# Kernel tuning notes

Measured on AMD Instinct MI355X. Metric: run time of the kernel, lower is better.

## Reference

```python
import jax, jax.numpy as jnp
import numpy as np

B, C, T, N = 8, 128, 12, 4096
E_HALF = 131072
EPS = 1e-5


def _linear_params(key, fan_in, fan_out):
    kw, kb = jax.random.split(key)
    bound = 1.0 / np.sqrt(fan_in)
    W = jax.random.uniform(kw, (fan_in, fan_out), jnp.float32, -bound, bound)
    b = jax.random.uniform(kb, (fan_out,), jnp.float32, -bound, bound)
    return W, b


def setup_inputs() -> dict:
    key = jax.random.key(0)
    ks = jax.random.split(key, 10)
    h_in = jax.random.normal(ks[0], (B, C, T, N), jnp.float32)
    # symmetric edge list: random pairs + reverses + self loops
    u = jax.random.randint(ks[1], (E_HALF,), 0, N, jnp.int32)
    v = jax.random.randint(ks[2], (E_HALF,), 0, N, jnp.int32)
    loops = jnp.arange(N, dtype=jnp.int32)
    row = jnp.concatenate([u, v, loops])
    col = jnp.concatenate([v, u, loops])
    edge_index = jnp.stack([row, col])  # [2, E]
    Wq, bq = _linear_params(ks[3], C, C)
    Wk, bk = _linear_params(ks[4], C, C)
    Wv, bv = _linear_params(ks[5], C, C)
    W1, b1 = _linear_params(ks[6], 2 * C, 4 * C)
    W2, b2 = _linear_params(ks[7], 4 * C, C)
    W3, b3 = _linear_params(ks[8], C, 1)
    return dict(h_in=h_in, edge_index=edge_index, Wq=Wq, bq=bq, Wk=Wk, bk=bk,
                Wv=Wv, bv=bv, W1=W1, b1=b1, W2=W2, b2=b2, W3=W3, b3=b3)


def _masked_instance_norm(x, mask_f):
    # stats over the non-self-loop edges only (matching torch, where the MLP
    # only sees edge_index[:, non_self_loop_mask])
    cnt = mask_f.sum()
    mean = (x * mask_f).sum(0) / cnt
    var = (((x - mean) ** 2) * mask_f).sum(0) / cnt
    return (x - mean) / jnp.sqrt(var + EPS)


def _forward(h_in, edge_index, Wq, bq, Wk, bk, Wv, bv, W1, b1, W2, b2, W3, b3):
    # ---- TemporalAttention ----
    x = jnp.transpose(h_in, (0, 3, 2, 1))  # [B, N, T, C]
    q = x @ Wq + bq
    k = x @ Wk + bk
    v = x @ Wv + bv
    scores = jnp.einsum('bntc,bnsc->bnts', q, k) / (C ** 0.5)
    attn = jax.nn.softmax(scores, axis=-1)
    weighted = jnp.einsum('bnts,bnsc->bntc', attn, v)
    emb = weighted.sum(axis=2)          # [B, N, C]
    emb_mean = emb.mean(axis=0)         # [N, C]

    # ---- ExtractorMLP on non-self-loop edges ----
    row, col = edge_index[0], edge_index[1]
    self_loop = row == col
    mask_f = (~self_loop).astype(emb_mean.dtype)[:, None]  # [E, 1]
    f12 = jnp.concatenate([emb_mean[row], emb_mean[col]], axis=-1)  # [E, 2C]
    h = jax.nn.relu(_masked_instance_norm(f12 @ W1 + b1, mask_f))
    h = jax.nn.relu(_masked_instance_norm(h @ W2 + b2, mask_f))
    logits = h @ W3 + b3                 # [E, 1]

    # concrete_sample, eval mode (deterministic)
    att = jax.nn.sigmoid(logits)
    all_att = jnp.where(self_loop[:, None], 1.0, att)  # [E, 1]

    # ---- transpose + reorder_like: match each edge with its reverse ----
    M = jnp.max(edge_index) + 1
    fwd_key = row * M + col
    rev_key = col * M + row
    order = jnp.argsort(fwd_key)
    pos = jnp.searchsorted(fwd_key[order], rev_key)
    perm = order[pos]                    # index of reverse edge
    edge_att = (all_att + all_att[perm]) * 0.5
    return edge_att


def reference(h_in, edge_index, Wq, bq, Wk, bk, Wv, bv, W1, b1, W2, b2, W3, b3):
    return _forward(h_in, edge_index, Wq, bq, Wk, bk, Wv, bv, W1, b1, W2, b2, W3, b3)
```

## Files before the change

kernel.cpp:

```cpp
#include <hip/hip_runtime.h>
#include <hip/hip_bf16.h>

#define CC     128
#define TT     12
#define NNODE  4096
#define NE     266240
#define EHALF  131072
#define F1     512
#define EPS    1e-5f
#define RSQRTC 0.08838834764831845f
#define LOG2E  1.4426950408889634f
#define EBG    48
#define NBLKG2 5547
#define NF2B   87
#define ST     40

#define O_XWM   0ull
#define O_ICNT  524288ull
#define O_CNT   524416ull
#define O_T     528512ull
#define O_S     528640ull
#define O_T2    545024ull
#define O_GTB   561664ull
#define O_W0B   569856ull
#define O_WC1   569920ull
#define O_WC2   635456ull
#define O_B1C   700992ull
#define O_M1    701504ull
#define O_IS1   702016ull
#define O_M2    702528ull
#define O_AW    702656ull
#define O_W2T   702784ull
#define O_PB    735552ull
#define O_QB    1784128ull
#define O_PART  2832704ull
#define O_PART2 4252736ull
#define O_Z2    4275008ull

typedef __attribute__((ext_vector_type(8))) short bf16x8;
typedef __attribute__((ext_vector_type(4))) float f32x4;

__device__ inline float bfbits2f(unsigned int v) { return __uint_as_float(v << 16); }
__device__ inline unsigned short f2bf(float x) {
  union { __hip_bfloat16 h; unsigned short u; } cv;
  cv.h = __float2bfloat16(x);
  return cv.u;
}
__device__ inline float f4get(const float4& v, int k) {
  return k == 0 ? v.x : k == 1 ? v.y : k == 2 ? v.z : v.w;
}

__global__ __launch_bounds__(256) void k_setup(
    const float* __restrict__ Wq, const float* __restrict__ bq,
    const float* __restrict__ Wk, const float* __restrict__ Wv,
    const float* __restrict__ bv, const float* __restrict__ W1,
    const float* __restrict__ b1, const float* __restrict__ W2,
    const int* __restrict__ row, const int* __restrict__ col,
    unsigned short* __restrict__ Gtb, unsigned short* __restrict__ w0b,
    float* __restrict__ Wc1, float* __restrict__ Wc2, float* __restrict__ b1c,
    unsigned short* __restrict__ W2T, int* __restrict__ cnt, int* __restrict__ icnt) {
  __shared__ float wvr[CC];
  __shared__ int h[NNODE];
  const int blk = blockIdx.x, tid = threadIdx.x;
  if (blk < 128) {
    if (tid < 128) {
      int i = blk, j = tid;
      float acc = 0.f;
      for (int co = 0; co < CC; ++co) acc = fmaf(Wq[i*CC+co], Wk[j*CC+co], acc);
      Gtb[j*CC + i] = f2bf(acc);
      if (j == 0) {
        float a = 0.f;
        for (int co = 0; co < CC; ++co) a = fmaf(Wk[i*CC+co], bq[co], a);
        w0b[i] = f2bf(a);
      }
    }
  } else if (blk < 256) {
    const int c = blk - 128;
    if (tid < CC) wvr[tid] = Wv[(size_t)c*CC + tid];
    __syncthreads();
    for (int hh = 0; hh < 2; ++hh) {
      int f = hh*256 + tid;
      float a1 = 0.f, a2 = 0.f;
      for (int j = 0; j < CC; ++j) {
        float wv = wvr[j];
        a1 = fmaf(wv, W1[(size_t)j*F1 + f], a1);
        a2 = fmaf(wv, W1[(size_t)(CC + j)*F1 + f], a2);
      }
      Wc1[(size_t)c*F1 + f] = a1;
      Wc2[(size_t)c*F1 + f] = a2;
    }
    if (c == 0) {
      for (int hh = 0; hh < 2; ++hh) {
        int f = hh*256 + tid;
        float s = b1[f];
        for (int j = 0; j < CC; ++j)
          s = fmaf(12.f*bv[j], W1[(size_t)j*F1 + f] + W1[(size_t)(CC + j)*F1 + f], s);
        b1c[f] = s;
      }
    }
  } else if (blk < 384) {
    const int n = blk - 256;
    for (int k = tid; k < F1; k += 256)
      W2T[(size_t)n*F1 + k] = f2bf(W2[(size_t)k*CC + n]);
  } else {
    for (int i = tid; i < NNODE; i += 256) h[i] = 0;
    __syncthreads();
    int lc = 0;
    const int base = (blk - 384) << 12;
    for (int i = tid; i < 4096; i += 256) {
      int e = base + i;
      int r = row[e], c = col[e];
      if (r != c) { atomicAdd(&h[r], 1); ++lc; }
    }
    #pragma unroll
    for (int d = 1; d < 64; d <<= 1) lc += __shfl_xor(lc, d);
    __syncthreads();
    for (int i = tid; i < NNODE; i += 256) { int v = h[i]; if (v) atomicAdd(&cnt[i], v); }
    if ((tid & 63) == 0) atomicAdd(icnt, lc);
  }
}

__global__ __launch_bounds__(512, 6) void k_attn(
    const float* __restrict__ h_in,
    const unsigned short* __restrict__ Gtb,
    const unsigned short* __restrict__ w0b,
    float* __restrict__ xwm) {
  __shared__ unsigned short xs[96*128];
  __shared__ unsigned short ys[97*128];
  const int tid = threadIdx.x;
  const int b  = blockIdx.x & 7;
  const int n0 = (blockIdx.x >> 3) << 3;

  const int w = tid >> 6, lane = tid & 63;
  const int l15 = lane & 15, l4 = lane >> 4;
  const int wm = w & 3, wg = w >> 2;

  bf16x8 gf[4][2];
  #pragma unroll
  for (int kt = 0; kt < 4; ++kt)
    #pragma unroll
    for (int mt = 0; mt < 2; ++mt)
      gf[kt][mt] = *(const bf16x8*)(Gtb + (size_t)((wm<<5) + (mt<<4) + l15)*CC + (kt<<5) + (l4<<3));

  {
    if (tid < 16) {
      uint4 wv = *(const uint4*)(w0b + (tid << 3));
      *(uint4*)((char*)ys + 96*256 + (tid << 4)) = wv;
    }
    #pragma unroll
    for (int k = 0; k < 3; ++k) {
      int p = tid + (k << 9);
      int half = p & 1;
      int q = p >> 1;
      int t = q % 12;
      int c2 = q / 12;
      const float* g = h_in + (((size_t)b*CC + 2*c2)*TT + t)*NNODE + n0 + half*4;
      float4 a0 = *(const float4*)g;
      float4 a1 = *(const float4*)(g + (size_t)TT*NNODE);
      #pragma unroll
      for (int i = 0; i < 4; ++i) {
        int r = (half*4 + i)*TT + t;
        unsigned byte = ((unsigned)r << 8) + (((unsigned)(c2*4)) ^ (((unsigned)(r & 7)) << 4));
        *(unsigned*)((char*)xs + byte) = (unsigned)f2bf(f4get(a0, i)) |
                                         ((unsigned)f2bf(f4get(a1, i)) << 16);
      }
    }
  }
  __syncthreads();

  {
    f32x4 acc[2][3];
    #pragma unroll
    for (int mt = 0; mt < 2; ++mt)
      #pragma unroll
      for (int nt = 0; nt < 3; ++nt) acc[mt][nt] = (f32x4){0.f,0.f,0.f,0.f};

    #pragma unroll
    for (int kt = 0; kt < 4; ++kt) {
      bf16x8 bfr[3];
      #pragma unroll
      for (int nt = 0; nt < 3; ++nt) {
        int rr = wg*48 + nt*16 + l15;
        unsigned byte = ((unsigned)rr << 8) +
                        (((unsigned)((kt<<6) + (l4<<4))) ^ (((unsigned)(rr & 7)) << 4));
        bfr[nt] = *(const bf16x8*)((const char*)xs + byte);
      }
      #pragma unroll
      for (int mt = 0; mt < 2; ++mt)
        #pragma unroll
        for (int nt = 0; nt < 3; ++nt)
          acc[mt][nt] = __builtin_amdgcn_mfma_f32_16x16x32_bf16(gf[kt][mt], bfr[nt], acc[mt][nt], 0, 0, 0);
    }
    #pragma unroll
    for (int mt = 0; mt < 2; ++mt)
      #pragma unroll
      for (int nt = 0; nt < 3; ++nt) {
        int rr = wg*48 + nt*16 + l15;
        ushort4 v;
        v.x = f2bf(acc[mt][nt][0]); v.y = f2bf(acc[mt][nt][1]);
        v.z = f2bf(acc[mt][nt][2]); v.w = f2bf(acc[mt][nt][3]);
        unsigned cb = (unsigned)((wm<<6) + (mt<<5) + (l4<<3));
        unsigned byte = ((unsigned)rr << 8) + (cb ^ (((unsigned)(rr & 7)) << 4));
        *(ushort4*)((char*)ys + byte) = v;
      }
  }
  __syncthreads();

  {
    const int rb = w*TT;
    const bool sval = (l15 < TT);
    const int rr  = rb + (sval ? l15 : 0);
    const int rra = sval ? (rb + l15) : 96;
    f32x4 sa = (f32x4){0.f,0.f,0.f,0.f};
    #pragma unroll
    for (int kt = 0; kt < 4; ++kt) {
      unsigned kb = (unsigned)((kt<<6) + (l4<<4));
      unsigned byteA = ((unsigned)rra << 8) + (kb ^ (((unsigned)(rra & 7)) << 4));
      unsigned byteB = ((unsigned)rr  << 8) + (kb ^ (((unsigned)(rr  & 7)) << 4));
      bf16x8 afr = *(const bf16x8*)((const char*)ys + byteA);
      bf16x8 bfr = *(const bf16x8*)((const char*)xs + byteB);
      sa = __builtin_amdgcn_mfma_f32_16x16x32_bf16(afr, bfr, sa, 0, 0, 0);
    }
    float dv = __shfl(sa[0], 48 + l15);
    float p[4];
    #pragma unroll
    for (int r = 0; r < 4; ++r) {
      float t1 = sval ? (sa[r] + dv) * RSQRTC : -1e30f;
      float e = exp2f(t1 * LOG2E);
      float s = e;
      s += __shfl_xor(s, 1);
      s += __shfl_xor(s, 2);
      s += __shfl_xor(s, 4);
      s += __shfl_xor(s, 8);
      p[r] = e / s;
    }
    float wpart = (l4 < 3) ? (p[0] + p[1] + p[2] + p[3]) : 0.f;
    wpart += __shfl_xor(wpart, 16);
    wpart += __shfl_xor(wpart, 32);
    float xw0 = 0.f, xw1 = 0.f;
    #pragma unroll
    for (int s = 0; s < TT; ++s) {
      float wv = __shfl(wpart, s);
      int r2 = rb + s;
      unsigned byte = ((unsigned)r2 << 8) +
                      (((unsigned)(lane << 2)) ^ (((unsigned)(r2 & 7)) << 4));
      unsigned xp = *(const unsigned*)((const char*)xs + byte);
      xw0 = fmaf(wv, bfbits2f(xp & 0xffffu), xw0);
      xw1 = fmaf(wv, bfbits2f(xp >> 16), xw1);
    }
    unsafeAtomicAdd(&xwm[(size_t)(n0 + w)*CC + (lane << 1)],     xw0 * 0.125f);
    unsafeAtomicAdd(&xwm[(size_t)(n0 + w)*CC + (lane << 1) + 1], xw1 * 0.125f);
  }
}

__global__ __launch_bounds__(256) void k_ST2(const float* __restrict__ xwm,
    const int* __restrict__ row, const int* __restrict__ col,
    const int* __restrict__ cnt, float* __restrict__ S,
    float* __restrict__ T2, float* __restrict__ t) {
  __shared__ unsigned short XT[128*ST];
  __shared__ unsigned short YT[128*ST];
  __shared__ float tl[128];
  const int tid = threadIdx.x;
  const int w = tid >> 6, lane = tid & 63, l15 = lane & 15, l4 = lane >> 4;
  const int j = tid & 31, fi = tid >> 5;
  const int f0 = fi << 4;
  f32x4 acc[2][8];
  #pragma unroll
  for (int mt = 0; mt < 2; ++mt)
    #pragma unroll
    for (int nt = 0; nt < 8; ++nt) acc[mt][nt] = (f32x4){0.f,0.f,0.f,0.f};

  if (blockIdx.x < 512) {
    const int ebase = blockIdx.x << 9;
    for (int bt = 0; bt < 16; ++bt) {
      const int e = ebase + (bt << 5) + j;
      const int r = row[e], c = col[e];
      const bool msk = (r != c);
      const float* xr = xwm + (size_t)r*CC + f0;
      const float* xc = xwm + (size_t)c*CC + f0;
      float4 xv[4], yv[4];
      #pragma unroll
      for (int u = 0; u < 4; ++u) { xv[u] = *(const float4*)(xr + 4*u); yv[u] = *(const float4*)(xc + 4*u); }
      __syncthreads();
      #pragma unroll
      for (int u = 0; u < 16; ++u) {
        float xvv = f4get(xv[u >> 2], u & 3);
        float yvv = f4get(yv[u >> 2], u & 3);
        XT[(f0+u)*ST + j] = f2bf(xvv);
        YT[(f0+u)*ST + j] = msk ? f2bf(yvv) : (unsigned short)0;
      }
      __syncthreads();
      bf16x8 af[2];
      #pragma unroll
      for (int mt = 0; mt < 2; ++mt)
        af[mt] = *(const bf16x8*)&XT[((((w<<1)+mt)<<4) + l15)*ST + (l4<<3)];
      #pragma unroll
      for (int nt = 0; nt < 8; ++nt) {
        bf16x8 bf_ = *(const bf16x8*)&YT[(((nt<<4) + l15))*ST + (l4<<3)];
        acc[0][nt] = __builtin_amdgcn_mfma_f32_16x16x32_bf16(af[0], bf_, acc[0][nt], 0, 0, 0);
        acc[1][nt] = __builtin_amdgcn_mfma_f32_16x16x32_bf16(af[1], bf_, acc[1][nt], 0, 0, 0);
      }
    }
    #pragma unroll
    for (int mt = 0; mt < 2; ++mt)
      #pragma unroll
      for (int nt = 0; nt < 8; ++nt)
        #pragma unroll
        for (int reg = 0; reg < 4; ++reg) {
          int a = (((w<<1)+mt)<<4) + (l4<<2) + reg;
          int b = (nt<<4) + l15;
          unsafeAtomicAdd(&S[a*128 + b], acc[mt][nt][reg]);
        }
  } else {
    if (tid < 128) tl[tid] = 0.f;
    float tloc[16];
    #pragma unroll
    for (int u = 0; u < 16; ++u) tloc[u] = 0.f;
    const int nbase = (blockIdx.x - 512) << 7;
    for (int bt = 0; bt < 4; ++bt) {
      const int n = nbase + (bt << 5) + j;
      const float cw = (float)cnt[n];
      const float* xr = xwm + (size_t)n*CC + f0;
      float4 xv[4];
      #pragma unroll
      for (int u = 0; u < 4; ++u) xv[u] = *(const float4*)(xr + 4*u);
      __syncthreads();
      #pragma unroll
      for (int u = 0; u < 16; ++u) {
        float xvv = f4get(xv[u >> 2], u & 3);
        float yvv = cw * xvv;
        XT[(f0+u)*ST + j] = f2bf(xvv);
        YT[(f0+u)*ST + j] = f2bf(yvv);
        tloc[u] += yvv;
      }
      __syncthreads();
      bf16x8 af[2];
      #pragma unroll
      for (int mt = 0; mt < 2; ++mt)
        af[mt] = *(const bf16x8*)&XT[((((w<<1)+mt)<<4) + l15)*ST + (l4<<3)];
      #pragma unroll
      for (int nt = 0; nt < 8; ++nt) {
        bf16x8 bf_ = *(const bf16x8*)&YT[(((nt<<4) + l15))*ST + (l4<<3)];
        acc[0][nt] = __builtin_amdgcn_mfma_f32_16x16x32_bf16(af[0], bf_, acc[0][nt], 0, 0, 0);
        acc[1][nt] = __builtin_amdgcn_mfma_f32_16x16x32_bf16(af[1], bf_, acc[1][nt], 0, 0, 0);
      }
    }
    #pragma unroll
    for (int u = 0; u < 16; ++u) atomicAdd(&tl[f0 + u], tloc[u]);
    #pragma unroll
    for (int mt = 0; mt < 2; ++mt)
      #pragma unroll
      for (int nt = 0; nt < 8; ++nt)
        #pragma unroll
        for (int reg = 0; reg < 4; ++reg) {
          int a = (((w<<1)+mt)<<4) + (l4<<2) + reg;
          int b = (nt<<4) + l15;
          unsafeAtomicAdd(&T2[a*128 + b], acc[mt][nt][reg]);
        }
    __syncthreads();
    if (tid < 128) unsafeAtomicAdd(&t[tid], tl[tid]);
  }
}

__global__ __launch_bounds__(128) void k_stats(const float* __restrict__ S,
    const float* __restrict__ T2, const float* __restrict__ Wc1,
    const float* __restrict__ Wc2, const float* __restrict__ b1c,
    const float* __restrict__ t, const int* __restrict__ icnt,
    float* __restrict__ m1, float* __restrict__ is1) {
  __shared__ float w1c[128], w2c[128];
  __shared__ float redq[2], redt1[2], redt2[2];
  const int f = blockIdx.x, a = threadIdx.x;
  w1c[a] = Wc1[(size_t)a*F1 + f];
  w2c[a] = Wc2[(size_t)a*F1 + f];
  __syncthreads();
  float v1 = 0.f, v2 = 0.f, v3 = 0.f;
  const float* Sr = S + a*128;
  const float* Tr = T2 + a*128;
  for (int b = 0; b < 128; b += 4) {
    float4 sv = *(const float4*)(Sr + b);
    float4 tv = *(const float4*)(Tr + b);
    float4 w1v = *(const float4*)&w1c[b];
    float4 w2v = *(const float4*)&w2c[b];
    #pragma unroll
    for (int u = 0; u < 4; ++u) {
      v1 = fmaf(f4get(sv, u), f4get(w2v, u), v1);
      v2 = fmaf(f4get(tv, u), f4get(w1v, u), v2);
      v3 = fmaf(f4get(tv, u), f4get(w2v, u), v3);
    }
  }
  float pa  = w1c[a]*(v2 + 2.f*v1) + w2c[a]*v3;
  float ta1 = t[a]*w1c[a];
  float ta2 = t[a]*w2c[a];
  #pragma unroll
  for (int d = 1; d < 64; d <<= 1) {
    pa  += __shfl_xor(pa, d);
    ta1 += __shfl_xor(ta1, d);
    ta2 += __shfl_xor(ta2, d);
  }
  if ((a & 63) == 0) { redq[a>>6] = pa; redt1[a>>6] = ta1; redt2[a>>6] = ta2; }
  __syncthreads();
  if (a == 0) {
    float cntf = (float)(*icnt);
    float bb = b1c[f];
    float sumq = redq[0] + redq[1];
    float st1 = redt1[0] + redt1[1];
    float st2 = redt2[0] + redt2[1];
    float w2tot = sumq + 2.f*bb*(st1 + st2) + cntf*bb*bb;
    float w1tot = st1 + st2 + cntf*bb;
    float m = w1tot / cntf;
    m1[f] = m;
    is1[f] = rsqrtf(w2tot/cntf - m*m + EPS);
  }
}

__global__ __launch_bounds__(256) void k_pq(const float* __restrict__ xwm,
    const float* __restrict__ Wc1, const float* __restrict__ Wc2,
    const float* __restrict__ b1c, const float* __restrict__ m1,
    const float* __restrict__ is1,
    unsigned short* __restrict__ Pb, unsigned short* __restrict__ Qb) {
  __shared__ float em[4][CC];
  const int tid = threadIdx.x;
  const int n0 = blockIdx.x << 2;
  for (int i = tid; i < 4*CC; i += 256)
    em[i >> 7][i & 127] = xwm[(size_t)(n0 + (i >> 7))*CC + (i & 127)];
  __syncthreads();
  for (int half = 0; half < 2; ++half) {
    const int f = half*256 + tid;
    const float mm = m1[f], ii = is1[f], bb = b1c[f];
    for (int nn = 0; nn < 4; ++nn) {
      float ap = bb, aq = 0.f;
      for (int c = 0; c < CC; ++c) {
        float e = em[nn][c];
        ap = fmaf(e, Wc1[(size_t)c*F1 + f], ap);
        aq = fmaf(e, Wc2[(size_t)c*F1 + f], aq);
      }
      Pb[(size_t)(n0+nn)*F1 + f] = f2bf(ap * ii);
      Qb[(size_t)(n0+nn)*F1 + f] = f2bf((aq - mm) * ii);
    }
  }
}

__global__ __launch_bounds__(512, 6) void k_gemm(const unsigned short* __restrict__ Pb,
    const unsigned short* __restrict__ Qb, const int* __restrict__ row,
    const int* __restrict__ col,
    const unsigned short* __restrict__ W2T, const float* __restrict__ b2,
    unsigned short* __restrict__ z2, float* __restrict__ part) {
  __shared__ unsigned short h1s[EBG*F1];
  __shared__ int rS[EBG], cS[EBG]; __shared__ float mk[EBG];
  __shared__ float cstat[256];
  const int tid = threadIdx.x;
  const int bid = blockIdx.x;
  const int e0 = bid * EBG;
  const int w = tid >> 6, lane = tid & 63;
  const int wn0 = w << 4;
  const int l15 = lane & 15, l4 = lane >> 4;
  if (tid < EBG) {
    int e = e0 + tid;
    bool valid = e < NE;
    int r = valid ? row[e] : 0, c = valid ? col[e] : 0;
    rS[tid] = r; cS[tid] = c; mk[tid] = (valid && r != c) ? 1.f : 0.f;
  }
  __syncthreads();

  {
    int jj[6], cc[6];
    #pragma unroll
    for (int s = 0; s < 6; ++s) {
      int i = tid + (s << 9);
      jj[s] = i >> 6; cc[s] = i & 63;
    }
    uint4 pv[6], qv[6];
    #pragma unroll
    for (int s = 0; s < 6; ++s) pv[s] = *(const uint4*)(Pb + (size_t)rS[jj[s]]*F1 + (cc[s] << 3));
    #pragma unroll
    for (int s = 0; s < 6; ++s) qv[s] = *(const uint4*)(Qb + (size_t)cS[jj[s]]*F1 + (cc[s] << 3));
    #pragma unroll
    for (int s = 0; s < 6; ++s) {
      unsigned out[4];
      #pragma unroll
      for (int q = 0; q < 4; ++q) {
        unsigned pu = (&pv[s].x)[q], qu = (&qv[s].x)[q];
        float ha = fmaxf(bfbits2f(pu & 0xffffu) + bfbits2f(qu & 0xffffu), 0.f);
        float hb = fmaxf(bfbits2f(pu >> 16)     + bfbits2f(qu >> 16),     0.f);
        out[q] = (unsigned)f2bf(ha) | ((unsigned)f2bf(hb) << 16);
      }
      unsigned byte = ((unsigned)jj[s] << 10) +
                      (((unsigned)(cc[s] << 4)) ^ (((unsigned)(jj[s] & 7)) << 4));
      *(uint4*)((char*)h1s + byte) = make_uint4(out[0], out[1], out[2], out[3]);
    }
  }
  __syncthreads();

  f32x4 acc[3];
  #pragma unroll
  for (int a = 0; a < 3; ++a) acc[a] = (f32x4){0.f,0.f,0.f,0.f};

  const unsigned short* w2p = W2T + (size_t)(wn0 + l15)*F1 + (l4 << 3);
  #pragma unroll
  for (int kt = 0; kt < 16; ++kt) {
    bf16x8 bfr = *(const bf16x8*)(w2p + (kt << 5));
    bf16x8 afr[3];
    #pragma unroll
    for (int mt = 0; mt < 3; ++mt) {
      int j = (mt << 4) + l15;
      unsigned byte = ((unsigned)j << 10) + (((unsigned)(kt*64 + l4*16)) ^ ((j & 7) << 4));
      afr[mt] = *(const bf16x8*)((const char*)h1s + byte);
    }
    #pragma unroll
    for (int mt = 0; mt < 3; ++mt)
      acc[mt] = __builtin_amdgcn_mfma_f32_16x16x32_bf16(afr[mt], bfr, acc[mt], 0, 0, 0);
  }
  __syncthreads();

  float* z2s = (float*)&h1s[0];
  const int colg = wn0 + l15;
  {
    float bb = b2[colg];
    float sloc = 0.f, qloc = 0.f;
    #pragma unroll
    for (int mt = 0; mt < 3; ++mt) {
      f32x4 v = acc[mt];
      #pragma unroll
      for (int reg = 0; reg < 4; ++reg) {
        int j = (mt << 4) + (l4 << 2) + reg;
        float z = v[reg] + bb;
        float m = mk[j];
        sloc = fmaf(m, z, sloc);
        qloc = fmaf(m*z, z, qloc);
        z2s[j*132 + colg] = z;
      }
    }
    sloc += __shfl_xor(sloc, 16); sloc += __shfl_xor(sloc, 32);
    qloc += __shfl_xor(qloc, 16); qloc += __shfl_xor(qloc, 32);
    if (l4 == 0) { cstat[colg] = sloc; cstat[128 + colg] = qloc; }
  }
  __syncthreads();

  #pragma unroll
  for (int p = 0; p < 2; ++p) {
    int idx = (p << 12) + (tid << 3);
    if (idx < EBG*CC) {
      int j = idx >> 7, c = idx & 127;
      if (e0 + j < NE) {
        const float* src = &z2s[j*132 + c];
        float4 v0 = *(const float4*)src;
        float4 v1 = *(const float4*)(src + 4);
        uint4 o;
        o.x = (unsigned)f2bf(v0.x) | ((unsigned)f2bf(v0.y) << 16);
        o.y = (unsigned)f2bf(v0.z) | ((unsigned)f2bf(v0.w) << 16);
        o.z = (unsigned)f2bf(v1.x) | ((unsigned)f2bf(v1.y) << 16);
        o.w = (unsigned)f2bf(v1.z) | ((unsigned)f2bf(v1.w) << 16);
        *(uint4*)(z2 + (size_t)e0*CC + idx) = o;
      }
    }
  }
  if (tid < 256) part[(size_t)bid*256 + tid] = cstat[tid];
}

__global__ __launch_bounds__(256) void k_fin2a(const float* __restrict__ part,
                                               float* __restrict__ part2) {
  const int g = blockIdx.x, tid = threadIdx.x;
  float s = 0.f;
  for (int r = 0; r < 64; ++r) {
    int b = g*64 + r;
    if (b < NBLKG2) s += part[(size_t)b*256 + tid];
  }
  part2[(size_t)g*256 + tid] = s;
}

__global__ __launch_bounds__(256) void k_fin2b(const float* __restrict__ part2,
    const int* __restrict__ icnt, const float* __restrict__ W3,
    float* __restrict__ m2, float* __restrict__ aw) {
  __shared__ float red[256];
  const int tid = threadIdx.x;
  float s = 0.f;
  for (int g = 0; g < NF2B; ++g) s += part2[(size_t)g*256 + tid];
  red[tid] = s;
  __syncthreads();
  if (tid < 128) {
    float cnt = (float)(*icnt);
    float m = red[tid] / cnt;
    m2[tid] = m;
    aw[tid] = rsqrtf(red[128 + tid]/cnt - m*m + EPS) * W3[tid];
  }
}

__global__ __launch_bounds__(256) void k_scoreout(const unsigned short* __restrict__ z2,
    const int* __restrict__ row, const int* __restrict__ col,
    const float* __restrict__ m2, const float* __restrict__ aw,
    const float* __restrict__ b3, float* __restrict__ out) {
  const int tid = threadIdx.x;
  if (blockIdx.x >= 2048) {
    int e = 2*EHALF + ((blockIdx.x - 2048) << 8) + tid;
    if (e < NE) out[e] = 1.f;
    return;
  }
  const int w = tid >> 6, lane = tid & 63;
  const int g = lane >> 4, sub = lane & 15;
  const int f0 = sub << 3;
  float mv[8], av[8];
  {
    float4 a0 = *(const float4*)(m2 + f0);
    float4 a1 = *(const float4*)(m2 + f0 + 4);
    float4 b0 = *(const float4*)(aw + f0);
    float4 b1 = *(const float4*)(aw + f0 + 4);
    #pragma unroll
    for (int u = 0; u < 4; ++u) { mv[u] = f4get(a0, u); mv[4+u] = f4get(a1, u); }
    #pragma unroll
    for (int u = 0; u < 4; ++u) { av[u] = f4get(b0, u); av[4+u] = f4get(b1, u); }
  }
  const float bb = b3[0];
  #pragma unroll
  for (int it = 0; it < 4; ++it) {
    const int e = (blockIdx.x << 6) + (w << 4) + (it << 2) + g;
    uint4 zva = *(const uint4*)(z2 + (size_t)e*CC + f0);
    uint4 zvb = *(const uint4*)(z2 + (size_t)(e + EHALF)*CC + f0);
    float aa = 0.f, ab = 0.f;
    #pragma unroll
    for (int u = 0; u < 4; ++u) {
      unsigned za = (&zva.x)[u], zb = (&zvb.x)[u];
      float a0 = bfbits2f(za & 0xffffu), a1 = bfbits2f(za >> 16);
      float b0 = bfbits2f(zb & 0xffffu), b1 = bfbits2f(zb >> 16);
      aa += (a0 > mv[2*u])   ? (a0 - mv[2*u])*av[2*u]     : 0.f;
      aa += (a1 > mv[2*u+1]) ? (a1 - mv[2*u+1])*av[2*u+1] : 0.f;
      ab += (b0 > mv[2*u])   ? (b0 - mv[2*u])*av[2*u]     : 0.f;
      ab += (b1 > mv[2*u+1]) ? (b1 - mv[2*u+1])*av[2*u+1] : 0.f;
    }
    #pragma unroll
    for (int d = 1; d < 16; d <<= 1) { aa += __shfl_xor(aa, d); ab += __shfl_xor(ab, d); }
    if (sub == 0) {
      int r = row[e], c = col[e];
      float o;
      if (r == c) o = 1.f;
      else {
        float s1 = 1.f/(1.f + expf(-(aa + bb)));
        float s2 = 1.f/(1.f + expf(-(ab + bb)));
        o = 0.5f*(s1 + s2);
      }
      out[e] = o;
      out[e + EHALF] = o;
    }
  }
}

extern "C" void kernel_launch(void* const* d_in, const int* in_sizes, int n_in,
                              void* d_out, int out_size, void* d_ws, size_t ws_size,
                              hipStream_t stream) {
  const float* h_in = (const float*)d_in[0];
  const int*   ei   = (const int*)d_in[1];
  const float* Wq = (const float*)d_in[2];
  const float* bq = (const float*)d_in[3];
  const float* Wk = (const float*)d_in[4];
  const float* bk = (const float*)d_in[5];  (void)bk;
  const float* Wv = (const float*)d_in[6];
  const float* bv = (const float*)d_in[7];
  const float* W1 = (const float*)d_in[8];
  const float* b1 = (const float*)d_in[9];
  const float* W2 = (const float*)d_in[10];
  const float* b2 = (const float*)d_in[11];
  const float* W3 = (const float*)d_in[12];
  const float* b3 = (const float*)d_in[13];
  float* ws = (float*)d_ws;
  float* out = (float*)d_out;
  const int* row = ei;
  const int* col = ei + NE;

  hipMemsetAsync(ws, 0, 561664ull * 4ull, stream);

  k_setup<<<448, 256, 0, stream>>>(Wq, bq, Wk, Wv, bv, W1, b1, W2, row, col,
                                   (unsigned short*)(ws+O_GTB), (unsigned short*)(ws+O_W0B),
                                   ws+O_WC1, ws+O_WC2, ws+O_B1C,
                                   (unsigned short*)(ws+O_W2T),
                                   (int*)(ws+O_CNT), (int*)(ws+O_ICNT));
  k_attn<<<4096, 512, 0, stream>>>(h_in, (const unsigned short*)(ws+O_GTB),
                                   (const unsigned short*)(ws+O_W0B), ws+O_XWM);
  k_ST2<<<544, 256, 0, stream>>>(ws+O_XWM, row, col, (const int*)(ws+O_CNT),
                                 ws+O_S, ws+O_T2, ws+O_T);
  k_stats<<<512, 128, 0, stream>>>(ws+O_S, ws+O_T2, ws+O_WC1, ws+O_WC2, ws+O_B1C,
                                   ws+O_T, (const int*)(ws+O_ICNT), ws+O_M1, ws+O_IS1);
  k_pq<<<1024, 256, 0, stream>>>(ws+O_XWM, ws+O_WC1, ws+O_WC2, ws+O_B1C,
                                 ws+O_M1, ws+O_IS1,
                                 (unsigned short*)(ws+O_PB), (unsigned short*)(ws+O_QB));
  k_gemm<<<NBLKG2, 512, 0, stream>>>((const unsigned short*)(ws+O_PB),
                                     (const unsigned short*)(ws+O_QB), row, col,
                                     (const unsigned short*)(ws+O_W2T), b2,
                                     (unsigned short*)(ws+O_Z2), ws+O_PART);
  k_fin2a<<<NF2B, 256, 0, stream>>>(ws+O_PART, ws+O_PART2);
  k_fin2b<<<1, 256, 0, stream>>>(ws+O_PART2, (const int*)(ws+O_ICNT), W3,
                                 ws+O_M2, ws+O_AW);
  k_scoreout<<<2064, 256, 0, stream>>>((const unsigned short*)(ws+O_Z2), row, col,
                                       ws+O_M2, ws+O_AW, b3, out);
}
```

Before: 403.9 us.

## Bucket edges by source-node group so edge GEMM gathers hit cache

Adds a counting-sort pass (per-bucket histogram in setup, scan, scatter) that builds a permutation grouping edges by row>>6. The edge GEMM processes edges in this permuted order so Pb row gathers come from a small set of nodes per block, and it writes z2 back to the original edge positions. It also hoists the attention input loads ahead of the bf16 conversion stores to overlap memory latency. The cost is two extra small launches, nondeterministic order within a bucket (which only affects partial-stat summation order), and scattered 256-byte z2 stores.

```diff
diff --git a/kernel.cpp b/kernel.cpp
--- a/kernel.cpp
+++ b/kernel.cpp
@@ -14,6 +14,7 @@
 #define NBLKG2 5547
 #define NF2B   87
 #define ST     40
+#define EPB    4160
 
 #define O_XWM   0ull
 #define O_ICNT  524288ull
@@ -21,21 +22,24 @@
 #define O_T     528512ull
 #define O_S     528640ull
 #define O_T2    545024ull
-#define O_GTB   561664ull
-#define O_W0B   569856ull
-#define O_WC1   569920ull
-#define O_WC2   635456ull
-#define O_B1C   700992ull
-#define O_M1    701504ull
-#define O_IS1   702016ull
-#define O_M2    702528ull
-#define O_AW    702656ull
+#define O_BCNT  561408ull
+#define O_GTB   561536ull
+#define O_W0B   569728ull
+#define O_WC1   569792ull
+#define O_WC2   635328ull
+#define O_B1C   700864ull
+#define O_M1    701376ull
+#define O_IS1   701888ull
+#define O_M2    702400ull
+#define O_AW    702528ull
+#define O_BCUR  702656ull
 #define O_W2T   702784ull
 #define O_PB    735552ull
 #define O_QB    1784128ull
-#define O_PART  2832704ull
-#define O_PART2 4252736ull
-#define O_Z2    4275008ull
+#define O_PERM  2832704ull
+#define O_PART  3098944ull
+#define O_PART2 4518976ull
+#define O_Z2    4541248ull
 
 typedef __attribute__((ext_vector_type(8))) short bf16x8;
 typedef __attribute__((ext_vector_type(4))) float f32x4;
@@ -58,9 +62,11 @@
     const int* __restrict__ row, const int* __restrict__ col,
     unsigned short* __restrict__ Gtb, unsigned short* __restrict__ w0b,
     float* __restrict__ Wc1, float* __restrict__ Wc2, float* __restrict__ b1c,
-    unsigned short* __restrict__ W2T, int* __restrict__ cnt, int* __restrict__ icnt) {
+    unsigned short* __restrict__ W2T, int* __restrict__ cnt, int* __restrict__ icnt,
+    int* __restrict__ bcnt) {
   __shared__ float wvr[CC];
   __shared__ int h[NNODE];
+  __shared__ int bh[64];
   const int blk = blockIdx.x, tid = threadIdx.x;
   if (blk < 128) {
     if (tid < 128) {
@@ -104,19 +110,54 @@
       W2T[(size_t)n*F1 + k] = f2bf(W2[(size_t)k*CC + n]);
   } else {
     for (int i = tid; i < NNODE; i += 256) h[i] = 0;
+    if (tid < 64) bh[tid] = 0;
     __syncthreads();
     int lc = 0;
-    const int base = (blk - 384) << 12;
-    for (int i = tid; i < 4096; i += 256) {
+    const int base = (blk - 384) * EPB;
+    for (int i = tid; i < EPB; i += 256) {
       int e = base + i;
       int r = row[e], c = col[e];
       if (r != c) { atomicAdd(&h[r], 1); ++lc; }
+      atomicAdd(&bh[r >> 6], 1);
     }
     #pragma unroll
     for (int d = 1; d < 64; d <<= 1) lc += __shfl_xor(lc, d);
     __syncthreads();
     for (int i = tid; i < NNODE; i += 256) { int v = h[i]; if (v) atomicAdd(&cnt[i], v); }
+    if (tid < 64 && bh[tid]) atomicAdd(&bcnt[tid], bh[tid]);
     if ((tid & 63) == 0) atomicAdd(icnt, lc);
+  }
+}
+
+__global__ void k_scan(const int* __restrict__ bcnt, int* __restrict__ bcur) {
+  const int tid = threadIdx.x;
+  int v = bcnt[tid];
+  int s = v;
+  #pragma unroll
+  for (int d = 1; d < 64; d <<= 1) { int o = __shfl_up(s, d); if (tid >= d) s += o; }
+  bcur[tid] = s - v;
+}
+
+__global__ __launch_bounds__(256) void k_scatter(const int* __restrict__ row,
+    int* __restrict__ bcur, int* __restrict__ perm) {
+  __shared__ int bh[64], bbase[64];
+  const int tid = threadIdx.x;
+  const int base = blockIdx.x * EPB;
+  if (tid < 64) bh[tid] = 0;
+  __syncthreads();
+  for (int i = tid; i < EPB; i += 256) atomicAdd(&bh[row[base + i] >> 6], 1);
+  __syncthreads();
+  if (tid < 64) {
+    int c = bh[tid];
+    bbase[tid] = c ? atomicAdd(&bcur[tid], c) : 0;
+    bh[tid] = 0;
+  }
+  __syncthreads();
+  for (int i = tid; i < EPB; i += 256) {
+    int e = base + i;
+    int b = row[e] >> 6;
+    int p = bbase[b] + atomicAdd(&bh[b], 1);
+    perm[p] = e;
   }
 }
 
@@ -147,22 +188,27 @@
       uint4 wv = *(const uint4*)(w0b + (tid << 3));
       *(uint4*)((char*)ys + 96*256 + (tid << 4)) = wv;
     }
+    float4 va[3], vb[3];
+    int ts[3], c2s[3], hs[3];
     #pragma unroll
     for (int k = 0; k < 3; ++k) {
       int p = tid + (k << 9);
-      int half = p & 1;
+      hs[k] = p & 1;
       int q = p >> 1;
-      int t = q % 12;
-      int c2 = q / 12;
-      const float* g = h_in + (((size_t)b*CC + 2*c2)*TT + t)*NNODE + n0 + half*4;
-      float4 a0 = *(const float4*)g;
-      float4 a1 = *(const float4*)(g + (size_t)TT*NNODE);
+      ts[k] = q % 12;
+      c2s[k] = q / 12;
+      const float* g = h_in + (((size_t)b*CC + 2*c2s[k])*TT + ts[k])*NNODE + n0 + hs[k]*4;
+      va[k] = *(const float4*)g;
+      vb[k] = *(const float4*)(g + (size_t)TT*NNODE);
+    }
+    #pragma unroll
+    for (int k = 0; k < 3; ++k) {
       #pragma unroll
       for (int i = 0; i < 4; ++i) {
-        int r = (half*4 + i)*TT + t;
-        unsigned byte = ((unsigned)r << 8) + (((unsigned)(c2*4)) ^ (((unsigned)(r & 7)) << 4));
-        *(unsigned*)((char*)xs + byte) = (unsigned)f2bf(f4get(a0, i)) |
-                                         ((unsigned)f2bf(f4get(a1, i)) << 16);
+        int r = (hs[k]*4 + i)*TT + ts[k];
+        unsigned byte = ((unsigned)r << 8) + (((unsigned)(c2s[k]*4)) ^ (((unsigned)(r & 7)) << 4));
+        *(unsigned*)((char*)xs + byte) = (unsigned)f2bf(f4get(va[k], i)) |
+                                         ((unsigned)f2bf(f4get(vb[k], i)) << 16);
       }
     }
   }
@@ -442,11 +488,11 @@
 
 __global__ __launch_bounds__(512, 6) void k_gemm(const unsigned short* __restrict__ Pb,
     const unsigned short* __restrict__ Qb, const int* __restrict__ row,
-    const int* __restrict__ col,
+    const int* __restrict__ col, const int* __restrict__ perm,
     const unsigned short* __restrict__ W2T, const float* __restrict__ b2,
     unsigned short* __restrict__ z2, float* __restrict__ part) {
   __shared__ unsigned short h1s[EBG*F1];
-  __shared__ int rS[EBG], cS[EBG]; __shared__ float mk[EBG];
+  __shared__ int rS[EBG], cS[EBG], eS[EBG]; __shared__ float mk[EBG];
   __shared__ float cstat[256];
   const int tid = threadIdx.x;
   const int bid = blockIdx.x;
@@ -455,10 +501,12 @@
   const int wn0 = w << 4;
   const int l15 = lane & 15, l4 = lane >> 4;
   if (tid < EBG) {
-    int e = e0 + tid;
-    bool valid = e < NE;
+    int i = e0 + tid;
+    bool valid = i < NE;
+    int e = valid ? perm[i] : 0;
     int r = valid ? row[e] : 0, c = valid ? col[e] : 0;
-    rS[tid] = r; cS[tid] = c; mk[tid] = (valid && r != c) ? 1.f : 0.f;
+    rS[tid] = r; cS[tid] = c; eS[tid] = valid ? e : -1;
+    mk[tid] = (valid && r != c) ? 1.f : 0.f;
   }
   __syncthreads();
 
@@ -541,7 +589,8 @@
     int idx = (p << 12) + (tid << 3);
     if (idx < EBG*CC) {
       int j = idx >> 7, c = idx & 127;
-      if (e0 + j < NE) {
+      int e = eS[j];
+      if (e >= 0) {
         const float* src = &z2s[j*132 + c];
         float4 v0 = *(const float4*)src;
         float4 v1 = *(const float4*)(src + 4);
@@ -550,7 +599,7 @@
         o.y = (unsigned)f2bf(v0.z) | ((unsigned)f2bf(v0.w) << 16);
         o.z = (unsigned)f2bf(v1.x) | ((unsigned)f2bf(v1.y) << 16);
         o.w = (unsigned)f2bf(v1.z) | ((unsigned)f2bf(v1.w) << 16);
-        *(uint4*)(z2 + (size_t)e0*CC + idx) = o;
+        *(uint4*)(z2 + (size_t)e*CC + c) = o;
       }
     }
   }
@@ -665,13 +714,16 @@
   const int* row = ei;
   const int* col = ei + NE;
 
-  hipMemsetAsync(ws, 0, 561664ull * 4ull, stream);
+  hipMemsetAsync(ws, 0, 561536ull * 4ull, stream);
 
   k_setup<<<448, 256, 0, stream>>>(Wq, bq, Wk, Wv, bv, W1, b1, W2, row, col,
                                    (unsigned short*)(ws+O_GTB), (unsigned short*)(ws+O_W0B),
                                    ws+O_WC1, ws+O_WC2, ws+O_B1C,
                                    (unsigned short*)(ws+O_W2T),
-                                   (int*)(ws+O_CNT), (int*)(ws+O_ICNT));
+                                   (int*)(ws+O_CNT), (int*)(ws+O_ICNT),
+                                   (int*)(ws+O_BCNT));
+  k_scan<<<1, 64, 0, stream>>>((const int*)(ws+O_BCNT), (int*)(ws+O_BCUR));
+  k_scatter<<<64, 256, 0, stream>>>(row, (int*)(ws+O_BCUR), (int*)(ws+O_PERM));
   k_attn<<<4096, 512, 0, stream>>>(h_in, (const unsigned short*)(ws+O_GTB),
                                    (const unsigned short*)(ws+O_W0B), ws+O_XWM);
   k_ST2<<<544, 256, 0, stream>>>(ws+O_XWM, row, col, (const int*)(ws+O_CNT),
@@ -683,6 +735,7 @@
                                  (unsigned short*)(ws+O_PB), (unsigned short*)(ws+O_QB));
   k_gemm<<<NBLKG2, 512, 0, stream>>>((const unsigned short*)(ws+O_PB),
                                      (const unsigned short*)(ws+O_QB), row, col,
+                                     (const int*)(ws+O_PERM),
                                      (const unsigned short*)(ws+O_W2T), b2,
                                      (unsigned short*)(ws+O_Z2), ws+O_PART);
   k_fin2a<<<NF2B, 256, 0, stream>>>(ws+O_PART, ws+O_PART2);
```

After: 413.8 us. +2.5%, slower.
